# Kernel optimization log

Hardware: AMD Instinct MI355X
Metric: run time of the kernel (lower is better)

Reference implementation:

```python
import jax, jax.numpy as jnp
import numpy as np

N_NODES = 50000


def _gcn_norm(edge_index, num_nodes):
    # Add self-loops (PyG GCNConv default) and compute symmetric norm.
    loops = jnp.arange(num_nodes, dtype=edge_index.dtype)
    src = jnp.concatenate([edge_index[0], loops])
    dst = jnp.concatenate([edge_index[1], loops])
    ones = jnp.ones(src.shape[0], dtype=jnp.float32)
    deg = jax.ops.segment_sum(ones, dst, num_segments=num_nodes)
    deg_inv_sqrt = jnp.where(deg > 0, jax.lax.rsqrt(jnp.maximum(deg, 1.0)), 0.0)
    norm = deg_inv_sqrt[src] * deg_inv_sqrt[dst]  # [E + N]
    return src, dst, norm


def _gcn_conv(x, src, dst, norm, W, b, num_nodes):
    xw = x @ W                               # [N, out]
    msg = xw[src] * norm[:, None]            # gather + scale  [E+N, out]
    out = jax.ops.segment_sum(msg, dst, num_segments=num_nodes)  # scatter-add
    return out + b


def setup_inputs() -> dict:
    key = jax.random.key(0)
    ks = jax.random.split(key, 10)
    d_in, d_h, d_out = 64, 64, 8
    n_edges = 800000
    x = jax.random.normal(ks[0], (N_NODES, d_in), dtype=jnp.float32)
    edge_index = jax.random.randint(ks[1], (2, n_edges), 0, N_NODES, dtype=jnp.int64)
    def w(k, fan_in, fan_out):
        return jax.random.normal(k, (fan_in, fan_out), dtype=jnp.float32) * (1.0 / np.sqrt(fan_in))
    return {
        "x": x,
        "edge_index": edge_index,
        "W0": w(ks[2], d_in, d_h), "b0": jnp.zeros((d_h,), jnp.float32),
        "W1": w(ks[3], d_h, d_h), "b1": jnp.zeros((d_h,), jnp.float32),
        "W2": w(ks[4], d_h, d_h), "b2": jnp.zeros((d_h,), jnp.float32),
        "linW": w(ks[5], d_h, d_out), "linb": jnp.zeros((d_out,), jnp.float32),
    }


def reference(x, edge_index, W0, b0, W1, b1, W2, b2, linW, linb):
    num_nodes = x.shape[0]
    src, dst, norm = _gcn_norm(edge_index, num_nodes)
    # 3 GCNConv layers, ReLU; dropout is identity at inference (training=False).
    for W, b in ((W0, b0), (W1, b1), (W2, b2)):
        x = jax.nn.relu(_gcn_conv(x, src, dst, norm, W, b, num_nodes))
    return x @ linW + linb
```

## Files before the change

kernel.cpp:

```cpp
#include <hip/hip_runtime.h>
#include <hip/hip_fp16.h>

#define TPB 256
#define CAP 16384
#define CAPSH 14
#define SC_BLOCKS 256
#define PB_BLOCKS 64
#define PB_CHUNK 784

typedef __attribute__((ext_vector_type(8))) float f32x8;
typedef __attribute__((ext_vector_type(8))) unsigned short u16x8;


__device__ __forceinline__ int ld_idx(const void* p, long long i, int is64) {
    return is64 ? (int)((const long long*)p)[i] : ((const int*)p)[i];
}

__device__ __forceinline__ ushort4 f4_to_h4(float4 v) {
    ushort4 r;
    r.x = __half_as_ushort(__float2half_rn(v.x));
    r.y = __half_as_ushort(__float2half_rn(v.y));
    r.z = __half_as_ushort(__float2half_rn(v.z));
    r.w = __half_as_ushort(__float2half_rn(v.w));
    return r;
}

__global__ __launch_bounds__(TPB) void p3_scatter(const void* __restrict__ ei,
                                                  long long E,
                                                  int* __restrict__ gcur,
                                                  int* __restrict__ pairs) {
    __shared__ int cnt[TPB];
    __shared__ int cur2[TPB];
    __shared__ int s_is64;
    int t = threadIdx.x;
    if (t < 64) {
        const unsigned int* w = (const unsigned int*)ei;
        unsigned long long m = __ballot(w[2 * t + 1] != 0u);
        if (t == 0) s_is64 = (m == 0ull) ? 1 : 0;
    }
    cnt[t] = 0;
    __syncthreads();
    const int is64 = s_is64;
    long long chunk = (E + SC_BLOCKS - 1) / SC_BLOCKS;
    long long s0 = (long long)blockIdx.x * chunk;
    long long s1 = (s0 + chunk < E) ? s0 + chunk : E;

    for (long long e = s0 + t; e < s1; e += TPB) {
        int d = ld_idx(ei, E + e, is64);
        atomicAdd(&cnt[d >> 8], 1);
    }
    __syncthreads();
    if (cnt[t]) cur2[t] = (t << CAPSH) + atomicAdd(&gcur[t], cnt[t]);
    __syncthreads();
    for (long long e = s0 + t; e < s1; e += TPB) {
        int sv = ld_idx(ei, e, is64);
        int d  = ld_idx(ei, E + e, is64);
        int pos = atomicAdd(&cur2[d >> 8], 1);
        pairs[pos] = (sv << 8) | (d & 255);
    }
}

__global__ __launch_bounds__(TPB) void p4_fill(const int* __restrict__ pairs,
                                               const int* __restrict__ gcur,
                                               const float* __restrict__ x,
                                               int2* __restrict__ meta,
                                               int* __restrict__ csr,
                                               ushort4* __restrict__ z0, int N) {
    __shared__ int ldeg[TPB];
    __shared__ int ssc[TPB];
    __shared__ int cur[TPB];
    __shared__ float fdis[TPB];
    int t = threadIdx.x;
    int b = blockIdx.x;
    int base = b << CAPSH;
    int ecnt = gcur[b];
    ldeg[t] = 0;
    __syncthreads();
    for (int e = base + t; e < base + ecnt; e += TPB)
        atomicAdd(&ldeg[pairs[e] & 255], 1);
    __syncthreads();
    int dv = ldeg[t];
    int pv = (dv + 7) & ~7;
    ssc[t] = pv;
    __syncthreads();
    for (int off = 1; off < TPB; off <<= 1) {
        int u = 0;
        if (t >= off) u = ssc[t - off];
        __syncthreads();
        ssc[t] += u;
        __syncthreads();
    }
    int o = base + ssc[t] - pv;
    cur[t] = o;
    float dd = rsqrtf((float)(dv + 1));
    fdis[t] = dd;
    int node = (b << 8) + t;
    if (node < N)
        meta[node] = make_int2((o << 8) | (pv >> 3), __float_as_int(dd));
    __syncthreads();
    for (int e = base + t; e < base + ecnt; e += TPB) {
        int p = pairs[e];
        int pos = atomicAdd(&cur[p & 255], 1);
        csr[pos] = p >> 8;
    }
    for (int e = o + dv; e < o + pv; ++e) csr[e] = N;

    int ni = t >> 4, c = t & 15;
    for (int p = 0; p < 16; ++p) {
        int nd = (b << 8) + p * 16 + ni;
        if (nd < N) {
            float dvv = fdis[p * 16 + ni];
            float4 h = ((const float4*)x)[(size_t)nd * 16 + c];
            float4 r = {h.x * dvv, h.y * dvv, h.z * dvv, h.w * dvv};
            z0[(size_t)nd * 16 + c] = f4_to_h4(r);
        }
    }
    if (b == 0 && t < 16) z0[(size_t)N * 16 + t] = make_ushort4(0, 0, 0, 0);
}

__global__ __launch_bounds__(TPB) void p5_perm(const int2* __restrict__ meta,
                                               int* __restrict__ perm,
                                               int N, int slots) {
    __shared__ int cnt[TPB];
    __shared__ int ssc[TPB];
    __shared__ int cur[TPB];
    int t = threadIdx.x;
    int s0 = blockIdx.x * PB_CHUNK;
    int s1 = s0 + PB_CHUNK < N ? s0 + PB_CHUNK : N;
    cnt[t] = 0;
    __syncthreads();
    for (int i = s0 + t; i < s1; i += TPB)
        atomicAdd(&cnt[meta[i].x & 255], 1);
    __syncthreads();
    int v = cnt[t];
    ssc[t] = v;
    __syncthreads();
    for (int off = 1; off < TPB; off <<= 1) {
        int u = 0;
        if (t >= off) u = ssc[t - off];
        __syncthreads();
        ssc[t] += u;
        __syncthreads();
    }
    cur[t] = s0 + ssc[t] - v;
    __syncthreads();
    for (int i = s0 + t; i < s1; i += TPB) {
        int pos = atomicAdd(&cur[meta[i].x & 255], 1);
        perm[pos] = i;
    }
    if (s0 < N && s1 == N)
        for (int i = N + t; i < slots; i += TPB) perm[i] = -1;
}

__device__ __forceinline__ f32x8 gather_rows(const u16x8* __restrict__ z8,
                                             const int* __restrict__ csr,
                                             int start, int nbatch, int c,
                                             f32x8 acc) {
    const int base = threadIdx.x & 56;
    int idx = (nbatch > 0) ? csr[start + c] : 0;
    for (int bt = 0; bt < nbatch; ++bt) {
        int nidx = (bt + 1 < nbatch) ? csr[start + (bt + 1) * 8 + c] : 0;
        #pragma unroll
        for (int k = 0; k < 8; ++k) {
            int s = __shfl(idx, base + k);
            u16x8 v = z8[(size_t)s * 8 + c];
            #pragma unroll
            for (int i = 0; i < 8; ++i)
                acc[i] += __half2float(__ushort_as_half(v[i]));
        }
        idx = nidx;
    }
    return acc;
}

__device__ __forceinline__ f32x8 shfl_mm8(f32x8 s, const float4* Ws4, int c) {
    const int base = threadIdx.x & 56;
    f32x8 u = {0.f, 0.f, 0.f, 0.f, 0.f, 0.f, 0.f, 0.f};
    #pragma unroll
    for (int q = 0; q < 8; ++q) {
        #pragma unroll
        for (int r = 0; r < 8; ++r) {
            float hv = __shfl(s[r], base + q);
            float4 w0 = Ws4[(q * 8 + r) * 16 + 2 * c];
            float4 w1 = Ws4[(q * 8 + r) * 16 + 2 * c + 1];
            u[0] = fmaf(hv, w0.x, u[0]);
            u[1] = fmaf(hv, w0.y, u[1]);
            u[2] = fmaf(hv, w0.z, u[2]);
            u[3] = fmaf(hv, w0.w, u[3]);
            u[4] = fmaf(hv, w1.x, u[4]);
            u[5] = fmaf(hv, w1.y, u[5]);
            u[6] = fmaf(hv, w1.z, u[6]);
            u[7] = fmaf(hv, w1.w, u[7]);
        }
    }
    return u;
}

__device__ __forceinline__ u16x8 f8_to_h8(f32x8 v) {
    u16x8 r;
    #pragma unroll
    for (int i = 0; i < 8; ++i)
        r[i] = __half_as_ushort(__float2half_rn(v[i]));
    return r;
}

__global__ __launch_bounds__(TPB) void layer_mm(const u16x8* __restrict__ z,
                                                const int* __restrict__ csr,
                                                const int2* __restrict__ meta,
                                                const int* __restrict__ perm,
                                                const float* __restrict__ b,
                                                const float* __restrict__ W,
                                                u16x8* __restrict__ zout, int n) {
    __shared__ float Ws[64 * 64];
    int t = threadIdx.x;
    float4* Ws4 = (float4*)Ws;
    const float4* W4g = (const float4*)W;
    #pragma unroll
    for (int i = 0; i < 4; ++i) Ws4[t + i * TPB] = W4g[t + i * TPB];

    if (blockIdx.x == 0 && t < 8) {
        u16x8 zz = {0, 0, 0, 0, 0, 0, 0, 0};
        zout[(size_t)n * 8 + t] = zz;
    }

    int wave = t >> 6, lane = t & 63;
    int g = lane >> 3, c = lane & 7;
    int node = perm[blockIdx.x * 32 + wave * 8 + g];
    f32x8 s = {0.f, 0.f, 0.f, 0.f, 0.f, 0.f, 0.f, 0.f};
    float dv = 0.f;
    if (node >= 0) {
        int2 m = meta[node];
        int start = ((unsigned)m.x) >> 8;
        int nbatch = m.x & 255;
        dv = __int_as_float(m.y);
        u16x8 v = z[(size_t)node * 8 + c];
        #pragma unroll
        for (int i = 0; i < 8; ++i) s[i] = __half2float(__ushort_as_half(v[i]));
        s = gather_rows(z, csr, start, nbatch, c, s);
    }
    __syncthreads();
    f32x8 u = shfl_mm8(s, Ws4, c);
    if (node >= 0) {
        float4 b0 = ((const float4*)b)[2 * c];
        float4 b1 = ((const float4*)b)[2 * c + 1];
        f32x8 r;
        r[0] = fmaxf(fmaf(dv, u[0], b0.x), 0.f) * dv;
        r[1] = fmaxf(fmaf(dv, u[1], b0.y), 0.f) * dv;
        r[2] = fmaxf(fmaf(dv, u[2], b0.z), 0.f) * dv;
        r[3] = fmaxf(fmaf(dv, u[3], b0.w), 0.f) * dv;
        r[4] = fmaxf(fmaf(dv, u[4], b1.x), 0.f) * dv;
        r[5] = fmaxf(fmaf(dv, u[5], b1.y), 0.f) * dv;
        r[6] = fmaxf(fmaf(dv, u[6], b1.z), 0.f) * dv;
        r[7] = fmaxf(fmaf(dv, u[7], b1.w), 0.f) * dv;
        zout[(size_t)node * 8 + c] = f8_to_h8(r);
    }
}

__global__ __launch_bounds__(TPB) void layer_final(const u16x8* __restrict__ z,
                                                   const int* __restrict__ csr,
                                                   const int2* __restrict__ meta,
                                                   const int* __restrict__ perm,
                                                   const float* __restrict__ b,
                                                   const float* __restrict__ W,
                                                   const float* __restrict__ Wl,
                                                   const float* __restrict__ bl,
                                                   float* __restrict__ out, int n) {
    __shared__ float Ws[64 * 64];
    __shared__ float Wls[64 * 8];
    __shared__ float bls[8];
    int t = threadIdx.x;
    float4* Ws4 = (float4*)Ws;
    const float4* W4g = (const float4*)W;
    #pragma unroll
    for (int i = 0; i < 4; ++i) Ws4[t + i * TPB] = W4g[t + i * TPB];
    if (t < 128) ((float4*)Wls)[t] = ((const float4*)Wl)[t];
    if (t < 8) bls[t] = bl[t];

    int wave = t >> 6, lane = t & 63;
    int g = lane >> 3, c = lane & 7;
    int node = perm[blockIdx.x * 32 + wave * 8 + g];
    f32x8 s = {0.f, 0.f, 0.f, 0.f, 0.f, 0.f, 0.f, 0.f};
    float dv = 0.f;
    if (node >= 0) {
        int2 m = meta[node];
        int start = ((unsigned)m.x) >> 8;
        int nbatch = m.x & 255;
        dv = __int_as_float(m.y);
        u16x8 v = z[(size_t)node * 8 + c];
        #pragma unroll
        for (int i = 0; i < 8; ++i) s[i] = __half2float(__ushort_as_half(v[i]));
        s = gather_rows(z, csr, start, nbatch, c, s);
    }
    __syncthreads();
    f32x8 u = shfl_mm8(s, Ws4, c);
    float4 b0 = ((const float4*)b)[2 * c];
    float4 b1 = ((const float4*)b)[2 * c + 1];
    f32x8 h;
    h[0] = fmaxf(fmaf(dv, u[0], b0.x), 0.f);
    h[1] = fmaxf(fmaf(dv, u[1], b0.y), 0.f);
    h[2] = fmaxf(fmaf(dv, u[2], b0.z), 0.f);
    h[3] = fmaxf(fmaf(dv, u[3], b0.w), 0.f);
    h[4] = fmaxf(fmaf(dv, u[4], b1.x), 0.f);
    h[5] = fmaxf(fmaf(dv, u[5], b1.y), 0.f);
    h[6] = fmaxf(fmaf(dv, u[6], b1.z), 0.f);
    h[7] = fmaxf(fmaf(dv, u[7], b1.w), 0.f);

    const int base = threadIdx.x & 56;
    float acc = bls[c];
    #pragma unroll
    for (int q = 0; q < 8; ++q) {
        #pragma unroll
        for (int r = 0; r < 8; ++r) {
            float hv = __shfl(h[r], base + q);
            acc = fmaf(hv, Wls[(q * 8 + r) * 8 + c], acc);
        }
    }
    if (node >= 0) out[(size_t)node * 8 + c] = acc;
}

extern "C" void kernel_launch(void* const* d_in, const int* in_sizes, int n_in,
                              void* d_out, int out_size, void* d_ws, size_t ws_size,
                              hipStream_t stream) {
    const float* x  = (const float*)d_in[0];
    const void*  ei = d_in[1];
    const float* W0 = (const float*)d_in[2];
    const float* b0 = (const float*)d_in[3];
    const float* W1 = (const float*)d_in[4];
    const float* b1 = (const float*)d_in[5];
    const float* W2 = (const float*)d_in[6];
    const float* b2 = (const float*)d_in[7];
    const float* Wl = (const float*)d_in[8];
    const float* bl = (const float*)d_in[9];

    const long long E = in_sizes[1] / 2;
    const int dh = in_sizes[3];
    const int din = in_sizes[2] / dh;
    const int N = in_sizes[0] / din;
    const int nb = (N + 255) >> 8;
    const int gL = (N + 31) / 32;
    const int slots = gL * 32;

    char* ws = (char*)d_ws;
    size_t off = 0;
    auto alloc = [&](size_t bytes) -> char* {
        char* r = ws + off;
        off += (bytes + 255) & ~(size_t)255;
        return r;
    };
    int*   gcur    = (int*)  alloc(1024);
    int2*  meta    = (int2*) alloc((size_t)N * 8);
    int*   perm    = (int*)  alloc((size_t)slots * 4);
    int*   pairs   = (int*)  alloc((size_t)nb * CAP * 4);
    int*   csr     = (int*)  alloc((size_t)nb * CAP * 4);
    u16x8* zbA     = (u16x8*)alloc((size_t)(N + 1) * 64 * 2);
    u16x8* zbB     = (u16x8*)alloc((size_t)(N + 1) * 64 * 2);

    hipMemsetAsync(gcur, 0, 256 * sizeof(int), stream);
    p3_scatter<<<SC_BLOCKS, TPB, 0, stream>>>(ei, E, gcur, pairs);
    p4_fill<<<nb, TPB, 0, stream>>>(pairs, gcur, x, meta, csr,
                                    (ushort4*)zbA, N);
    p5_perm<<<PB_BLOCKS, TPB, 0, stream>>>(meta, perm, N, slots);

    layer_mm<<<gL, TPB, 0, stream>>>(zbA, csr, meta, perm, b0, W0, zbB, N);
    layer_mm<<<gL, TPB, 0, stream>>>(zbB, csr, meta, perm, b1, W1, zbA, N);
    layer_final<<<gL, TPB, 0, stream>>>(zbA, csr, meta, perm, b2, W2, Wl, bl,
                                        (float*)d_out, N);
}
```

Before: 189.5 us.

## Process two nodes per 8-lane group in layer kernels to reuse weights

Each 8-lane group now handles two destination nodes instead of one, so blocks cover 64 nodes and the grid is halved. Neighbor gathers for both nodes are interleaved in one loop to expose more memory-level parallelism, and the shared-memory weight reads in the 64x64 and final projections are reused across both nodes. The cost is higher register pressure, possible lower occupancy, and load imbalance when the two nodes have different degrees.

```diff
diff --git a/kernel.cpp b/kernel.cpp
--- a/kernel.cpp
+++ b/kernel.cpp
@@ -152,48 +152,58 @@
         for (int i = N + t; i < slots; i += TPB) perm[i] = -1;
 }
 
-__device__ __forceinline__ f32x8 gather_rows(const u16x8* __restrict__ z8,
-                                             const int* __restrict__ csr,
-                                             int start, int nbatch, int c,
-                                             f32x8 acc) {
+__device__ __forceinline__ void gather8(const u16x8* __restrict__ z8,
+                                        int idx, int c, int base, f32x8& acc) {
+    #pragma unroll
+    for (int k = 0; k < 8; ++k) {
+        int s = __shfl(idx, base + k);
+        u16x8 v = z8[(size_t)s * 8 + c];
+        #pragma unroll
+        for (int i = 0; i < 8; ++i)
+            acc[i] += __half2float(__ushort_as_half(v[i]));
+    }
+}
+
+__device__ __forceinline__ void gather_pair(const u16x8* __restrict__ z8,
+                                            const int* __restrict__ csr,
+                                            int sa, int nba, int sb, int nbb,
+                                            int c, f32x8& aa, f32x8& ab) {
     const int base = threadIdx.x & 56;
-    int idx = (nbatch > 0) ? csr[start + c] : 0;
-    for (int bt = 0; bt < nbatch; ++bt) {
-        int nidx = (bt + 1 < nbatch) ? csr[start + (bt + 1) * 8 + c] : 0;
-        #pragma unroll
-        for (int k = 0; k < 8; ++k) {
-            int s = __shfl(idx, base + k);
-            u16x8 v = z8[(size_t)s * 8 + c];
-            #pragma unroll
-            for (int i = 0; i < 8; ++i)
-                acc[i] += __half2float(__ushort_as_half(v[i]));
-        }
-        idx = nidx;
-    }
-    return acc;
-}
-
-__device__ __forceinline__ f32x8 shfl_mm8(f32x8 s, const float4* Ws4, int c) {
+    int btmax = nba > nbb ? nba : nbb;
+    int idxa = (nba > 0) ? csr[sa + c] : 0;
+    int idxb = (nbb > 0) ? csr[sb + c] : 0;
+    for (int bt = 0; bt < btmax; ++bt) {
+        int nidxa = (bt + 1 < nba) ? csr[sa + (bt + 1) * 8 + c] : 0;
+        int nidxb = (bt + 1 < nbb) ? csr[sb + (bt + 1) * 8 + c] : 0;
+        if (bt < nba) gather8(z8, idxa, c, base, aa);
+        if (bt < nbb) gather8(z8, idxb, c, base, ab);
+        idxa = nidxa;
+        idxb = nidxb;
+    }
+}
+
+__device__ __forceinline__ void shfl_mm8_pair(const f32x8& sa, const f32x8& sb,
+                                              const float4* Ws4, int c,
+                                              f32x8& ua, f32x8& ub) {
     const int base = threadIdx.x & 56;
-    f32x8 u = {0.f, 0.f, 0.f, 0.f, 0.f, 0.f, 0.f, 0.f};
     #pragma unroll
     for (int q = 0; q < 8; ++q) {
         #pragma unroll
         for (int r = 0; r < 8; ++r) {
-            float hv = __shfl(s[r], base + q);
             float4 w0 = Ws4[(q * 8 + r) * 16 + 2 * c];
             float4 w1 = Ws4[(q * 8 + r) * 16 + 2 * c + 1];
-            u[0] = fmaf(hv, w0.x, u[0]);
-            u[1] = fmaf(hv, w0.y, u[1]);
-            u[2] = fmaf(hv, w0.z, u[2]);
-            u[3] = fmaf(hv, w0.w, u[3]);
-            u[4] = fmaf(hv, w1.x, u[4]);
-            u[5] = fmaf(hv, w1.y, u[5]);
-            u[6] = fmaf(hv, w1.z, u[6]);
-            u[7] = fmaf(hv, w1.w, u[7]);
+            float ha = __shfl(sa[r], base + q);
+            float hb = __shfl(sb[r], base + q);
+            ua[0] = fmaf(ha, w0.x, ua[0]);  ub[0] = fmaf(hb, w0.x, ub[0]);
+            ua[1] = fmaf(ha, w0.y, ua[1]);  ub[1] = fmaf(hb, w0.y, ub[1]);
+            ua[2] = fmaf(ha, w0.z, ua[2]);  ub[2] = fmaf(hb, w0.z, ub[2]);
+            ua[3] = fmaf(ha, w0.w, ua[3]);  ub[3] = fmaf(hb, w0.w, ub[3]);
+            ua[4] = fmaf(ha, w1.x, ua[4]);  ub[4] = fmaf(hb, w1.x, ub[4]);
+            ua[5] = fmaf(ha, w1.y, ua[5]);  ub[5] = fmaf(hb, w1.y, ub[5]);
+            ua[6] = fmaf(ha, w1.z, ua[6]);  ub[6] = fmaf(hb, w1.z, ub[6]);
+            ua[7] = fmaf(ha, w1.w, ua[7]);  ub[7] = fmaf(hb, w1.w, ub[7]);
         }
     }
-    return u;
 }
 
 __device__ __forceinline__ u16x8 f8_to_h8(f32x8 v) {
@@ -201,6 +211,20 @@
     #pragma unroll
     for (int i = 0; i < 8; ++i)
         r[i] = __half_as_ushort(__float2half_rn(v[i]));
+    return r;
+}
+
+__device__ __forceinline__ f32x8 relu_scale(const f32x8& u, float dv,
+                                            float4 b0, float4 b1, float post) {
+    f32x8 r;
+    r[0] = fmaxf(fmaf(dv, u[0], b0.x), 0.f) * post;
+    r[1] = fmaxf(fmaf(dv, u[1], b0.y), 0.f) * post;
+    r[2] = fmaxf(fmaf(dv, u[2], b0.z), 0.f) * post;
+    r[3] = fmaxf(fmaf(dv, u[3], b0.w), 0.f) * post;
+    r[4] = fmaxf(fmaf(dv, u[4], b1.x), 0.f) * post;
+    r[5] = fmaxf(fmaf(dv, u[5], b1.y), 0.f) * post;
+    r[6] = fmaxf(fmaf(dv, u[6], b1.z), 0.f) * post;
+    r[7] = fmaxf(fmaf(dv, u[7], b1.w), 0.f) * post;
     return r;
 }
 
@@ -225,35 +249,40 @@
 
     int wave = t >> 6, lane = t & 63;
     int g = lane >> 3, c = lane & 7;
-    int node = perm[blockIdx.x * 32 + wave * 8 + g];
-    f32x8 s = {0.f, 0.f, 0.f, 0.f, 0.f, 0.f, 0.f, 0.f};
-    float dv = 0.f;
-    if (node >= 0) {
-        int2 m = meta[node];
-        int start = ((unsigned)m.x) >> 8;
-        int nbatch = m.x & 255;
-        dv = __int_as_float(m.y);
-        u16x8 v = z[(size_t)node * 8 + c];
-        #pragma unroll
-        for (int i = 0; i < 8; ++i) s[i] = __half2float(__ushort_as_half(v[i]));
-        s = gather_rows(z, csr, start, nbatch, c, s);
-    }
-    __syncthreads();
-    f32x8 u = shfl_mm8(s, Ws4, c);
-    if (node >= 0) {
-        float4 b0 = ((const float4*)b)[2 * c];
-        float4 b1 = ((const float4*)b)[2 * c + 1];
-        f32x8 r;
-        r[0] = fmaxf(fmaf(dv, u[0], b0.x), 0.f) * dv;
-        r[1] = fmaxf(fmaf(dv, u[1], b0.y), 0.f) * dv;
-        r[2] = fmaxf(fmaf(dv, u[2], b0.z), 0.f) * dv;
-        r[3] = fmaxf(fmaf(dv, u[3], b0.w), 0.f) * dv;
-        r[4] = fmaxf(fmaf(dv, u[4], b1.x), 0.f) * dv;
-        r[5] = fmaxf(fmaf(dv, u[5], b1.y), 0.f) * dv;
-        r[6] = fmaxf(fmaf(dv, u[6], b1.z), 0.f) * dv;
-        r[7] = fmaxf(fmaf(dv, u[7], b1.w), 0.f) * dv;
-        zout[(size_t)node * 8 + c] = f8_to_h8(r);
-    }
+    int s0 = blockIdx.x * 64 + wave * 16;
+    int na = perm[s0 + g];
+    int nb = perm[s0 + 8 + g];
+    f32x8 sa = {0.f, 0.f, 0.f, 0.f, 0.f, 0.f, 0.f, 0.f};
+    f32x8 sb = {0.f, 0.f, 0.f, 0.f, 0.f, 0.f, 0.f, 0.f};
+    float dva = 0.f, dvb = 0.f;
+    int sta = 0, nba = 0, stb = 0, nbb = 0;
+    if (na >= 0) {
+        int2 m = meta[na];
+        sta = ((unsigned)m.x) >> 8;
+        nba = m.x & 255;
+        dva = __int_as_float(m.y);
+        u16x8 v = z[(size_t)na * 8 + c];
+        #pragma unroll
+        for (int i = 0; i < 8; ++i) sa[i] = __half2float(__ushort_as_half(v[i]));
+    }
+    if (nb >= 0) {
+        int2 m = meta[nb];
+        stb = ((unsigned)m.x) >> 8;
+        nbb = m.x & 255;
+        dvb = __int_as_float(m.y);
+        u16x8 v = z[(size_t)nb * 8 + c];
+        #pragma unroll
+        for (int i = 0; i < 8; ++i) sb[i] = __half2float(__ushort_as_half(v[i]));
+    }
+    gather_pair(z, csr, sta, nba, stb, nbb, c, sa, sb);
+    __syncthreads();
+    f32x8 ua = {0.f, 0.f, 0.f, 0.f, 0.f, 0.f, 0.f, 0.f};
+    f32x8 ub = {0.f, 0.f, 0.f, 0.f, 0.f, 0.f, 0.f, 0.f};
+    shfl_mm8_pair(sa, sb, Ws4, c, ua, ub);
+    float4 b0 = ((const float4*)b)[2 * c];
+    float4 b1 = ((const float4*)b)[2 * c + 1];
+    if (na >= 0) zout[(size_t)na * 8 + c] = f8_to_h8(relu_scale(ua, dva, b0, b1, dva));
+    if (nb >= 0) zout[(size_t)nb * 8 + c] = f8_to_h8(relu_scale(ub, dvb, b0, b1, dvb));
 }
 
 __global__ __launch_bounds__(TPB) void layer_final(const u16x8* __restrict__ z,
@@ -278,44 +307,56 @@
 
     int wave = t >> 6, lane = t & 63;
     int g = lane >> 3, c = lane & 7;
-    int node = perm[blockIdx.x * 32 + wave * 8 + g];
-    f32x8 s = {0.f, 0.f, 0.f, 0.f, 0.f, 0.f, 0.f, 0.f};
-    float dv = 0.f;
-    if (node >= 0) {
-        int2 m = meta[node];
-        int start = ((unsigned)m.x) >> 8;
-        int nbatch = m.x & 255;
-        dv = __int_as_float(m.y);
-        u16x8 v = z[(size_t)node * 8 + c];
-        #pragma unroll
-        for (int i = 0; i < 8; ++i) s[i] = __half2float(__ushort_as_half(v[i]));
-        s = gather_rows(z, csr, start, nbatch, c, s);
-    }
-    __syncthreads();
-    f32x8 u = shfl_mm8(s, Ws4, c);
+    int s0 = blockIdx.x * 64 + wave * 16;
+    int na = perm[s0 + g];
+    int nb = perm[s0 + 8 + g];
+    f32x8 sa = {0.f, 0.f, 0.f, 0.f, 0.f, 0.f, 0.f, 0.f};
+    f32x8 sb = {0.f, 0.f, 0.f, 0.f, 0.f, 0.f, 0.f, 0.f};
+    float dva = 0.f, dvb = 0.f;
+    int sta = 0, nba = 0, stb = 0, nbb = 0;
+    if (na >= 0) {
+        int2 m = meta[na];
+        sta = ((unsigned)m.x) >> 8;
+        nba = m.x & 255;
+        dva = __int_as_float(m.y);
+        u16x8 v = z[(size_t)na * 8 + c];
+        #pragma unroll
+        for (int i = 0; i < 8; ++i) sa[i] = __half2float(__ushort_as_half(v[i]));
+    }
+    if (nb >= 0) {
+        int2 m = meta[nb];
+        stb = ((unsigned)m.x) >> 8;
+        nbb = m.x & 255;
+        dvb = __int_as_float(m.y);
+        u16x8 v = z[(size_t)nb * 8 + c];
+        #pragma unroll
+        for (int i = 0; i < 8; ++i) sb[i] = __half2float(__ushort_as_half(v[i]));
+    }
+    gather_pair(z, csr, sta, nba, stb, nbb, c, sa, sb);
+    __syncthreads();
+    f32x8 ua = {0.f, 0.f, 0.f, 0.f, 0.f, 0.f, 0.f, 0.f};
+    f32x8 ub = {0.f, 0.f, 0.f, 0.f, 0.f, 0.f, 0.f, 0.f};
+    shfl_mm8_pair(sa, sb, Ws4, c, ua, ub);
     float4 b0 = ((const float4*)b)[2 * c];
     float4 b1 = ((const float4*)b)[2 * c + 1];
-    f32x8 h;
-    h[0] = fmaxf(fmaf(dv, u[0], b0.x), 0.f);
-    h[1] = fmaxf(fmaf(dv, u[1], b0.y), 0.f);
-    h[2] = fmaxf(fmaf(dv, u[2], b0.z), 0.f);
-    h[3] = fmaxf(fmaf(dv, u[3], b0.w), 0.f);
-    h[4] = fmaxf(fmaf(dv, u[4], b1.x), 0.f);
-    h[5] = fmaxf(fmaf(dv, u[5], b1.y), 0.f);
-    h[6] = fmaxf(fmaf(dv, u[6], b1.z), 0.f);
-    h[7] = fmaxf(fmaf(dv, u[7], b1.w), 0.f);
-
-    const int base = threadIdx.x & 56;
-    float acc = bls[c];
+    f32x8 ha = relu_scale(ua, dva, b0, b1, 1.f);
+    f32x8 hb = relu_scale(ub, dvb, b0, b1, 1.f);
+
+    const int base = t & 56;
+    float acca = bls[c], accb = bls[c];
     #pragma unroll
     for (int q = 0; q < 8; ++q) {
         #pragma unroll
         for (int r = 0; r < 8; ++r) {
-            float hv = __shfl(h[r], base + q);
-            acc = fmaf(hv, Wls[(q * 8 + r) * 8 + c], acc);
+            float wv = Wls[(q * 8 + r) * 8 + c];
+            float va = __shfl(ha[r], base + q);
+            float vb = __shfl(hb[r], base + q);
+            acca = fmaf(va, wv, acca);
+            accb = fmaf(vb, wv, accb);
         }
     }
-    if (node >= 0) out[(size_t)node * 8 + c] = acc;
+    if (na >= 0) out[(size_t)na * 8 + c] = acca;
+    if (nb >= 0) out[(size_t)nb * 8 + c] = accb;
 }
 
 extern "C" void kernel_launch(void* const* d_in, const int* in_sizes, int n_in,
@@ -337,8 +378,8 @@
     const int din = in_sizes[2] / dh;
     const int N = in_sizes[0] / din;
     const int nb = (N + 255) >> 8;
-    const int gL = (N + 31) / 32;
-    const int slots = gL * 32;
+    const int gL = (N + 63) / 64;
+    const int slots = gL * 64;
 
     char* ws = (char*)d_ws;
     size_t off = 0;
```

Result: slower. 432.6 us (+128.3%).
